# Performance work log

Hardware: AMD Instinct MI355X
Metric: run time of the kernel (lower is better)

The kernel has to match this reference:

```python
import jax, jax.numpy as jnp
import numpy as np

DIM = 2048
HEADS = 16
B = 2
T = 2048


def setup_inputs() -> dict:
    key = jax.random.key(0)
    k_x, k_qkv, k_out, k_b = jax.random.split(key, 4)
    inv = DIM ** -0.5
    return {
        "x": jax.random.normal(k_x, (B, T, DIM), dtype=jnp.float32),
        "w_qkv": jax.random.normal(k_qkv, (DIM, 3 * DIM), dtype=jnp.float32) * inv,
        "w_out": jax.random.normal(k_out, (DIM, DIM), dtype=jnp.float32) * inv,
        "b_out": jnp.zeros((DIM,), dtype=jnp.float32),
    }


def reference(x, w_qkv, w_out, b_out):
    b, t, e = x.shape
    h = HEADS
    d = e // h
    scale = d ** -0.5
    qkv = x @ w_qkv                              # [b, t, 3e]
    q, k, v = jnp.split(qkv, 3, axis=-1)
    # [b, t, e] -> [b, h, t, d]
    q, k, v = (a.reshape(b, t, h, d).transpose(0, 2, 1, 3) for a in (q, k, v))
    dots = jnp.einsum("bhid,bhjd->bhij", q, k) * scale  # [b, h, t, t]
    causal_mask = jnp.triu(jnp.ones((t, t), dtype=bool), k=1)  # True where j > i
    dots = jnp.where(causal_mask[None, None, :, :], -jnp.inf, dots)
    attn = jax.nn.softmax(dots, axis=-1)
    out = jnp.einsum("bhij,bhjd->bhid", attn, v)  # [b, h, t, d]
    out = out.transpose(0, 2, 1, 3).reshape(b, t, e)
    return out @ w_out + b_out
```

## Files before the change

### kernel.cpp

```cpp
#include <hip/hip_runtime.h>
#include <stdint.h>

#define BATCH 2
#define TDIM 2048
#define EDIM 2048
#define NH 16
#define HD 128
#define E3 6144
#define MROWS 4096

typedef short v8bf __attribute__((ext_vector_type(8)));
typedef float v4f  __attribute__((ext_vector_type(4)));

typedef __attribute__((address_space(3))) uint8_t lds_u8;
typedef __attribute__((address_space(1))) uint8_t glb_u8;

__device__ __forceinline__ void gload16(const void* g, void* l) {
    __builtin_amdgcn_global_load_lds((const glb_u8*)g, (lds_u8*)l, 16, 0, 0);
}

__device__ __forceinline__ ushort f2bf(float f) {
    uint32_t u = __float_as_uint(f);
    return (ushort)((u + 0x7fffu + ((u >> 16) & 1u)) >> 16);
}

__global__ void cvtx_kernel(const float* __restrict__ in, ushort* __restrict__ out, int n) {
    int i = (blockIdx.x * 256 + threadIdx.x) * 4;
    const int stride = gridDim.x * 256 * 4;
    for (; i < n; i += stride) {
        const float4 v = *reinterpret_cast<const float4*>(in + i);
        ushort4 o = make_ushort4(f2bf(v.x), f2bf(v.y), f2bf(v.z), f2bf(v.w));
        *reinterpret_cast<ushort4*>(out + i) = o;
    }
}

__global__ void tcvt_kernel(const float* __restrict__ in, ushort* __restrict__ out, int R, int C) {
    __shared__ float t[32][33];
    const int tc = blockIdx.x * 32;
    const int tr = blockIdx.y * 32;
    const int tid = threadIdx.x;
    const int row = tid >> 3, c4 = (tid & 7) * 4;
    const float4 v = *reinterpret_cast<const float4*>(in + (size_t)(tr + row) * C + tc + c4);
    t[row][c4] = v.x; t[row][c4 + 1] = v.y; t[row][c4 + 2] = v.z; t[row][c4 + 3] = v.w;
    __syncthreads();
    const int oc = tid >> 3, r4 = (tid & 7) * 4;
    ushort4 o = make_ushort4(f2bf(t[r4][oc]), f2bf(t[r4 + 1][oc]),
                             f2bf(t[r4 + 2][oc]), f2bf(t[r4 + 3][oc]));
    *reinterpret_cast<ushort4*>(out + (size_t)(tc + oc) * R + tr + r4) = o;
}

__global__ void vtrans_kernel(const ushort* __restrict__ qkv, ushort* __restrict__ vt) {
    __shared__ ushort t[32][33];
    const int bh = blockIdx.z;
    const int b = bh >> 4, h = bh & 15;
    const int tr = blockIdx.x * 32;
    const int tc = blockIdx.y * 32;
    const int tid = threadIdx.x;
    const int row = tid >> 3, c4 = (tid & 7) * 4;
    const ushort4 v = *reinterpret_cast<const ushort4*>(
        qkv + (size_t)(b * TDIM + tr + row) * E3 + 2 * EDIM + h * HD + tc + c4);
    t[row][c4] = v.x; t[row][c4 + 1] = v.y; t[row][c4 + 2] = v.z; t[row][c4 + 3] = v.w;
    __syncthreads();
    const int oc = tid >> 3, r4 = (tid & 7) * 4;
    ushort4 o = make_ushort4(t[r4][oc], t[r4 + 1][oc], t[r4 + 2][oc], t[r4 + 3][oc]);
    *reinterpret_cast<ushort4*>(vt + (size_t)(bh * HD + tc + oc) * TDIM + tr + r4) = o;
}

template <int OUTF32>
__global__ void gemm_kernel(const ushort* __restrict__ A, const ushort* __restrict__ Bt,
                            void* __restrict__ Cv, const float* __restrict__ bias,
                            int Mdim, int Ndim, int Kdim) {
    __shared__ __align__(16) ushort As[128 * 64];
    __shared__ __align__(16) ushort Bs[128 * 64];
    const int tid = threadIdx.x;
    const int lane = tid & 63;
    const int wv = tid >> 6;
    const int l4 = lane >> 4, l16 = lane & 15;
    const int nbn = Ndim >> 7;
    const int nwg = (Mdim >> 7) * nbn;
    int bid = blockIdx.x;
    bid = (bid & 7) * (nwg >> 3) + (bid >> 3);
    const int bm = bid / nbn, bn = bid % nbn;
    const int wr = wv >> 1, wc = wv & 1;

    const ushort* Abase = A + (size_t)(bm * 128) * Kdim;
    const ushort* Bbase = Bt + (size_t)(bn * 128) * Kdim;

    v4f acc[4][4] = {};

    for (int k0 = 0; k0 < Kdim; k0 += 64) {
#pragma unroll
        for (int i = 0; i < 4; ++i) {
            const int c = i * 256 + tid;
            const int row = c >> 3;
            const int kc = (c & 7) ^ (row & 7);
            gload16(Abase + (size_t)row * Kdim + k0 + kc * 8, &As[(i * 256 + wv * 64) * 8]);
        }
#pragma unroll
        for (int i = 0; i < 4; ++i) {
            const int c = i * 256 + tid;
            const int row = c >> 3;
            const int kc = (c & 7) ^ (row & 7);
            gload16(Bbase + (size_t)row * Kdim + k0 + kc * 8, &Bs[(i * 256 + wv * 64) * 8]);
        }
        __syncthreads();
#pragma unroll
        for (int kk = 0; kk < 2; ++kk) {
            v8bf af[4], bfr[4];
#pragma unroll
            for (int m = 0; m < 4; ++m) {
                const int r = wr * 64 + m * 16 + l16;
                const int slot = (kk * 4 + l4) ^ (r & 7);
                af[m] = *reinterpret_cast<const v8bf*>(&As[r * 64 + slot * 8]);
            }
#pragma unroll
            for (int n = 0; n < 4; ++n) {
                const int r = wc * 64 + n * 16 + l16;
                const int slot = (kk * 4 + l4) ^ (r & 7);
                bfr[n] = *reinterpret_cast<const v8bf*>(&Bs[r * 64 + slot * 8]);
            }
#pragma unroll
            for (int m = 0; m < 4; ++m)
#pragma unroll
                for (int n = 0; n < 4; ++n)
                    acc[m][n] = __builtin_amdgcn_mfma_f32_16x16x32_bf16(af[m], bfr[n], acc[m][n], 0, 0, 0);
        }
        __syncthreads();
    }

    const int r0 = bm * 128 + wr * 64 + l4 * 4;
    const int c0 = bn * 128 + wc * 64 + l16;
    if (OUTF32) {
        float* C = (float*)Cv;
#pragma unroll
        for (int n = 0; n < 4; ++n) {
            const float bv = bias[c0 + n * 16];
#pragma unroll
            for (int m = 0; m < 4; ++m)
#pragma unroll
                for (int j = 0; j < 4; ++j)
                    C[(size_t)(r0 + m * 16 + j) * Ndim + c0 + n * 16] = acc[m][n][j] + bv;
        }
    } else {
        ushort* C = (ushort*)Cv;
#pragma unroll
        for (int n = 0; n < 4; ++n)
#pragma unroll
            for (int m = 0; m < 4; ++m)
#pragma unroll
                for (int j = 0; j < 4; ++j)
                    C[(size_t)(r0 + m * 16 + j) * Ndim + c0 + n * 16] = f2bf(acc[m][n][j]);
    }
}

__global__ __launch_bounds__(256, 2) void flash_kernel(const ushort* __restrict__ qkv,
                                                       const ushort* __restrict__ vt,
                                                       ushort* __restrict__ ao) {
    __shared__ __align__(16) ushort Kl[2][64 * 128];
    __shared__ __align__(16) ushort Vl[2][128 * 64];
    __shared__ __align__(16) ushort Pl[128 * 64];

    const int qt = (TDIM / 128 - 1) - blockIdx.x;
    const int h = blockIdx.y;
    const int b = blockIdx.z;
    const int tid = threadIdx.x;
    const int lane = tid & 63;
    const int wv = tid >> 6;
    const int l4 = lane >> 4, l16 = lane & 15;
    const int q0 = qt * 128;

    v8bf qf[2][4];
#pragma unroll
    for (int mg = 0; mg < 2; ++mg) {
        const ushort* qp = qkv + (size_t)(b * TDIM + q0 + wv * 32 + mg * 16 + l16) * E3 + h * HD + l4 * 8;
#pragma unroll
        for (int d0 = 0; d0 < 4; ++d0)
            qf[mg][d0] = *reinterpret_cast<const v8bf*>(qp + d0 * 32);
    }

    float mrun[2][4], lrun[2][4];
#pragma unroll
    for (int mg = 0; mg < 2; ++mg)
#pragma unroll
        for (int j = 0; j < 4; ++j) { mrun[mg][j] = -1e30f; lrun[mg][j] = 0.0f; }
    v4f oacc[2][8] = {};

    const ushort* kbase = qkv + (size_t)(b * TDIM) * E3 + EDIM + h * HD;
    const ushort* vbase = vt + (size_t)((b * 16 + h) * HD) * TDIM;
    const int nkt = 2 * qt + 2;

#define STAGE(BUF, KT)                                                                        \
    do {                                                                                      \
        _Pragma("unroll") for (int i = 0; i < 4; ++i) {                                       \
            const int c = i * 256 + tid;                                                      \
            const int row = c >> 4;                                                           \
            const int dc = (c & 15) ^ (row & 7);                                              \
            gload16(kbase + (size_t)((KT) * 64 + row) * E3 + dc * 8,                          \
                    &Kl[BUF][(i * 256 + wv * 64) * 8]);                                       \
        }                                                                                     \
        _Pragma("unroll") for (int i = 0; i < 4; ++i) {                                       \
            const int c = i * 256 + tid;                                                      \
            const int row = c >> 3;                                                           \
            const int jc = (c & 7) ^ (row & 7);                                               \
            gload16(vbase + (size_t)row * TDIM + (KT) * 64 + jc * 8,                          \
                    &Vl[BUF][(i * 256 + wv * 64) * 8]);                                       \
        }                                                                                     \
    } while (0)

    STAGE(0, 0);
    __syncthreads();
    int cur = 0;

    for (int kt = 0; kt < nkt; ++kt) {
        if (kt + 1 < nkt) STAGE(cur ^ 1, kt + 1);

        const ushort* Kb = &Kl[cur][0];
        const ushort* Vb = &Vl[cur][0];

        v4f s[2][4] = {};
#pragma unroll
        for (int d0 = 0; d0 < 4; ++d0) {
            v8bf kf[4];
#pragma unroll
            for (int kvn = 0; kvn < 4; ++kvn) {
                const int r = kvn * 16 + l16;
                const int slot = (d0 * 4 + l4) ^ (r & 7);
                kf[kvn] = *reinterpret_cast<const v8bf*>(&Kb[r * 128 + slot * 8]);
            }
#pragma unroll
            for (int mg = 0; mg < 2; ++mg)
#pragma unroll
                for (int kvn = 0; kvn < 4; ++kvn)
                    s[mg][kvn] = __builtin_amdgcn_mfma_f32_16x16x32_bf16(qf[mg][d0], kf[kvn], s[mg][kvn], 0, 0, 0);
        }

        float sv[2][4][4];
#pragma unroll
        for (int mg = 0; mg < 2; ++mg)
#pragma unroll
            for (int kvn = 0; kvn < 4; ++kvn)
#pragma unroll
                for (int j = 0; j < 4; ++j)
                    sv[mg][kvn][j] = s[mg][kvn][j] * 0.08838834764831845f;

        if (kt >= 2 * qt) {
#pragma unroll
            for (int mg = 0; mg < 2; ++mg) {
                const int rg = q0 + wv * 32 + mg * 16 + l4 * 4;
#pragma unroll
                for (int kvn = 0; kvn < 4; ++kvn) {
                    const int cg = kt * 64 + kvn * 16 + l16;
#pragma unroll
                    for (int j = 0; j < 4; ++j)
                        if (cg > rg + j) sv[mg][kvn][j] = -__builtin_inff();
                }
            }
        }

        float p[2][4][4];
#pragma unroll
        for (int mg = 0; mg < 2; ++mg) {
            float corr[4];
#pragma unroll
            for (int j = 0; j < 4; ++j) {
                float pm = fmaxf(fmaxf(sv[mg][0][j], sv[mg][1][j]), fmaxf(sv[mg][2][j], sv[mg][3][j]));
                pm = fmaxf(pm, __shfl_xor(pm, 1));
                pm = fmaxf(pm, __shfl_xor(pm, 2));
                pm = fmaxf(pm, __shfl_xor(pm, 4));
                pm = fmaxf(pm, __shfl_xor(pm, 8));
                const float mn = fmaxf(mrun[mg][j], pm);
                corr[j] = __expf(mrun[mg][j] - mn);
                mrun[mg][j] = mn;
            }
#pragma unroll
            for (int kvn = 0; kvn < 4; ++kvn)
#pragma unroll
                for (int j = 0; j < 4; ++j)
                    p[mg][kvn][j] = __expf(sv[mg][kvn][j] - mrun[mg][j]);
#pragma unroll
            for (int j = 0; j < 4; ++j)
                lrun[mg][j] = lrun[mg][j] * corr[j] + p[mg][0][j] + p[mg][1][j] + p[mg][2][j] + p[mg][3][j];
#pragma unroll
            for (int n = 0; n < 8; ++n)
#pragma unroll
                for (int j = 0; j < 4; ++j)
                    oacc[mg][n][j] *= corr[j];
        }

#pragma unroll
        for (int mg = 0; mg < 2; ++mg) {
            const int row = wv * 32 + mg * 16 + l4 * 4;
#pragma unroll
            for (int kvn = 0; kvn < 4; ++kvn) {
                const int cc = kvn * 2 + (l16 >> 3);
#pragma unroll
                for (int j = 0; j < 4; ++j) {
                    const int r = row + j;
                    Pl[r * 64 + ((cc ^ (r & 7)) * 8) + (l16 & 7)] = f2bf(p[mg][kvn][j]);
                }
            }
        }

#pragma unroll
        for (int kk = 0; kk < 2; ++kk) {
            v8bf pf[2];
#pragma unroll
            for (int mg = 0; mg < 2; ++mg) {
                const int r = wv * 32 + mg * 16 + l16;
                const int slot = (kk * 4 + l4) ^ (r & 7);
                pf[mg] = *reinterpret_cast<const v8bf*>(&Pl[r * 64 + slot * 8]);
            }
#pragma unroll
            for (int n = 0; n < 8; ++n) {
                const int dr = n * 16 + l16;
                const int slot = (kk * 4 + l4) ^ (dr & 7);
                v8bf vf = *reinterpret_cast<const v8bf*>(&Vb[dr * 64 + slot * 8]);
#pragma unroll
                for (int mg = 0; mg < 2; ++mg)
                    oacc[mg][n] = __builtin_amdgcn_mfma_f32_16x16x32_bf16(pf[mg], vf, oacc[mg][n], 0, 0, 0);
            }
        }
        __syncthreads();
        cur ^= 1;
    }
#undef STAGE

#pragma unroll
    for (int mg = 0; mg < 2; ++mg) {
        float inv[4];
#pragma unroll
        for (int j = 0; j < 4; ++j) {
            float l = lrun[mg][j];
            l += __shfl_xor(l, 1);
            l += __shfl_xor(l, 2);
            l += __shfl_xor(l, 4);
            l += __shfl_xor(l, 8);
            inv[j] = 1.0f / l;
        }
        ushort* aop = ao + (size_t)(b * TDIM + q0 + wv * 32 + mg * 16 + l4 * 4) * EDIM + h * HD + l16;
#pragma unroll
        for (int n = 0; n < 8; ++n)
#pragma unroll
            for (int j = 0; j < 4; ++j)
                aop[(size_t)j * EDIM + n * 16] = f2bf(oacc[mg][n][j] * inv[j]);
    }
}

extern "C" void kernel_launch(void* const* d_in, const int* in_sizes, int n_in,
                              void* d_out, int out_size, void* d_ws, size_t ws_size,
                              hipStream_t stream) {
    (void)in_sizes; (void)n_in; (void)out_size; (void)ws_size;
    const float* x     = (const float*)d_in[0];
    const float* w_qkv = (const float*)d_in[1];
    const float* w_out = (const float*)d_in[2];
    const float* b_out = (const float*)d_in[3];

    uint8_t* ws = (uint8_t*)d_ws;
    ushort* qkv   = (ushort*)(ws);
    ushort* woutT = (ushort*)(ws + 50331648u);
    ushort* xb    = (ushort*)(ws + 58720256u);
    ushort* wqkvT = (ushort*)(ws + 75497472u);
    ushort* vtb   = xb;
    ushort* ao    = wqkvT;

    cvtx_kernel<<<2048, 256, 0, stream>>>(x, xb, MROWS * EDIM);
    tcvt_kernel<<<dim3(E3 / 32, EDIM / 32), 256, 0, stream>>>(w_qkv, wqkvT, EDIM, E3);
    tcvt_kernel<<<dim3(EDIM / 32, EDIM / 32), 256, 0, stream>>>(w_out, woutT, EDIM, EDIM);

    gemm_kernel<0><<<(MROWS / 128) * (E3 / 128), 256, 0, stream>>>(
        xb, wqkvT, (void*)qkv, nullptr, MROWS, E3, EDIM);

    vtrans_kernel<<<dim3(TDIM / 32, HD / 32, BATCH * NH), 256, 0, stream>>>(qkv, vtb);

    flash_kernel<<<dim3(TDIM / 128, NH, BATCH), 256, 0, stream>>>(qkv, vtb, ao);

    gemm_kernel<1><<<(MROWS / 128) * (EDIM / 128), 256, 0, stream>>>(
        ao, woutT, d_out, b_out, MROWS, EDIM, EDIM);
}
```

Before: 298.8 us.

## Pair mirrored causal query tiles per block and use lazy softmax rescaling

Result: faster. 265.1 us (-11.3%).

```diff
diff --git a/kernel.cpp b/kernel.cpp
--- a/kernel.cpp
+++ b/kernel.cpp
@@ -160,22 +160,34 @@
     __shared__ __align__(16) ushort Vl[2][128 * 64];
     __shared__ __align__(16) ushort Pl[128 * 64];
 
-    const int qt = (TDIM / 128 - 1) - blockIdx.x;
+    const int xi = blockIdx.x;
+    const int ti = (xi & 1) ? (xi >> 1) : (15 - (xi >> 1));
     const int h = blockIdx.y;
     const int b = blockIdx.z;
     const int tid = threadIdx.x;
     const int lane = tid & 63;
     const int wv = tid >> 6;
     const int l4 = lane >> 4, l16 = lane & 15;
-    const int q0 = qt * 128;
+
+    const int rbs[2]  = {ti * 64 + wv * 16, TDIM - 64 * (ti + 1) + wv * 16};
+    const int diag[2] = {ti, 31 - ti};
+    const int nkt = 32 - ti;
 
     v8bf qf[2][4];
 #pragma unroll
     for (int mg = 0; mg < 2; ++mg) {
-        const ushort* qp = qkv + (size_t)(b * TDIM + q0 + wv * 32 + mg * 16 + l16) * E3 + h * HD + l4 * 8;
-#pragma unroll
-        for (int d0 = 0; d0 < 4; ++d0)
-            qf[mg][d0] = *reinterpret_cast<const v8bf*>(qp + d0 * 32);
+        const ushort* qp = qkv + (size_t)(b * TDIM + rbs[mg] + l16) * E3 + h * HD + l4 * 8;
+#pragma unroll
+        for (int d0 = 0; d0 < 4; ++d0) {
+            v8bf r = *reinterpret_cast<const v8bf*>(qp + d0 * 32);
+            v8bf o;
+#pragma unroll
+            for (int e = 0; e < 8; ++e) {
+                const float f = __uint_as_float(((uint32_t)(ushort)r[e]) << 16) * 0.08838834764831845f;
+                o[e] = (short)f2bf(f);
+            }
+            qf[mg][d0] = o;
+        }
     }
 
     float mrun[2][4], lrun[2][4];
@@ -187,7 +199,6 @@
 
     const ushort* kbase = qkv + (size_t)(b * TDIM) * E3 + EDIM + h * HD;
     const ushort* vbase = vt + (size_t)((b * 16 + h) * HD) * TDIM;
-    const int nkt = 2 * qt + 2;
 
 #define STAGE(BUF, KT)                                                                        \
     do {                                                                                      \
@@ -214,6 +225,7 @@
     for (int kt = 0; kt < nkt; ++kt) {
         if (kt + 1 < nkt) STAGE(cur ^ 1, kt + 1);
 
+        const bool act0 = (kt <= diag[0]);
         const ushort* Kb = &Kl[cur][0];
         const ushort* Vb = &Vl[cur][0];
 
@@ -228,67 +240,72 @@
                 kf[kvn] = *reinterpret_cast<const v8bf*>(&Kb[r * 128 + slot * 8]);
             }
 #pragma unroll
-            for (int mg = 0; mg < 2; ++mg)
-#pragma unroll
-                for (int kvn = 0; kvn < 4; ++kvn)
-                    s[mg][kvn] = __builtin_amdgcn_mfma_f32_16x16x32_bf16(qf[mg][d0], kf[kvn], s[mg][kvn], 0, 0, 0);
-        }
-
-        float sv[2][4][4];
-#pragma unroll
-        for (int mg = 0; mg < 2; ++mg)
+            for (int kvn = 0; kvn < 4; ++kvn) {
+                if (act0)
+                    s[0][kvn] = __builtin_amdgcn_mfma_f32_16x16x32_bf16(qf[0][d0], kf[kvn], s[0][kvn], 0, 0, 0);
+                s[1][kvn] = __builtin_amdgcn_mfma_f32_16x16x32_bf16(qf[1][d0], kf[kvn], s[1][kvn], 0, 0, 0);
+            }
+        }
+
+#pragma unroll
+        for (int mg = 0; mg < 2; ++mg) {
+            if (mg == 0 && !act0) continue;
+
+            float sv[4][4];
 #pragma unroll
             for (int kvn = 0; kvn < 4; ++kvn)
 #pragma unroll
                 for (int j = 0; j < 4; ++j)
-                    sv[mg][kvn][j] = s[mg][kvn][j] * 0.08838834764831845f;
-
-        if (kt >= 2 * qt) {
-#pragma unroll
-            for (int mg = 0; mg < 2; ++mg) {
-                const int rg = q0 + wv * 32 + mg * 16 + l4 * 4;
+                    sv[kvn][j] = s[mg][kvn][j];
+
+            if (kt == diag[mg]) {
+                const int rg = rbs[mg] + l4 * 4;
 #pragma unroll
                 for (int kvn = 0; kvn < 4; ++kvn) {
                     const int cg = kt * 64 + kvn * 16 + l16;
 #pragma unroll
                     for (int j = 0; j < 4; ++j)
-                        if (cg > rg + j) sv[mg][kvn][j] = -__builtin_inff();
+                        if (cg > rg + j) sv[kvn][j] = -__builtin_inff();
                 }
             }
-        }
-
-        float p[2][4][4];
-#pragma unroll
-        for (int mg = 0; mg < 2; ++mg) {
-            float corr[4];
+
+            float pm[4], dmax = -1e30f;
 #pragma unroll
             for (int j = 0; j < 4; ++j) {
-                float pm = fmaxf(fmaxf(sv[mg][0][j], sv[mg][1][j]), fmaxf(sv[mg][2][j], sv[mg][3][j]));
-                pm = fmaxf(pm, __shfl_xor(pm, 1));
-                pm = fmaxf(pm, __shfl_xor(pm, 2));
-                pm = fmaxf(pm, __shfl_xor(pm, 4));
-                pm = fmaxf(pm, __shfl_xor(pm, 8));
-                const float mn = fmaxf(mrun[mg][j], pm);
-                corr[j] = __expf(mrun[mg][j] - mn);
-                mrun[mg][j] = mn;
-            }
+                float m0 = fmaxf(fmaxf(sv[0][j], sv[1][j]), fmaxf(sv[2][j], sv[3][j]));
+                m0 = fmaxf(m0, __shfl_xor(m0, 1));
+                m0 = fmaxf(m0, __shfl_xor(m0, 2));
+                m0 = fmaxf(m0, __shfl_xor(m0, 4));
+                m0 = fmaxf(m0, __shfl_xor(m0, 8));
+                pm[j] = m0;
+                dmax = fmaxf(dmax, m0 - mrun[mg][j]);
+            }
+            if (!__all(dmax <= 8.0f)) {
+                float corr[4];
+#pragma unroll
+                for (int j = 0; j < 4; ++j) {
+                    const float mn = fmaxf(mrun[mg][j], pm[j]);
+                    corr[j] = __expf(mrun[mg][j] - mn);
+                    mrun[mg][j] = mn;
+                    lrun[mg][j] *= corr[j];
+                }
+#pragma unroll
+                for (int n = 0; n < 8; ++n)
+#pragma unroll
+                    for (int j = 0; j < 4; ++j)
+                        oacc[mg][n][j] *= corr[j];
+            }
+
+            float p[4][4];
 #pragma unroll
             for (int kvn = 0; kvn < 4; ++kvn)
 #pragma unroll
                 for (int j = 0; j < 4; ++j)
-                    p[mg][kvn][j] = __expf(sv[mg][kvn][j] - mrun[mg][j]);
+                    p[kvn][j] = __expf(sv[kvn][j] - mrun[mg][j]);
 #pragma unroll
             for (int j = 0; j < 4; ++j)
-                lrun[mg][j] = lrun[mg][j] * corr[j] + p[mg][0][j] + p[mg][1][j] + p[mg][2][j] + p[mg][3][j];
-#pragma unroll
-            for (int n = 0; n < 8; ++n)
-#pragma unroll
-                for (int j = 0; j < 4; ++j)
-                    oacc[mg][n][j] *= corr[j];
-        }
-
-#pragma unroll
-        for (int mg = 0; mg < 2; ++mg) {
+                lrun[mg][j] += p[0][j] + p[1][j] + p[2][j] + p[3][j];
+
             const int row = wv * 32 + mg * 16 + l4 * 4;
 #pragma unroll
             for (int kvn = 0; kvn < 4; ++kvn) {
@@ -296,7 +313,7 @@
 #pragma unroll
                 for (int j = 0; j < 4; ++j) {
                     const int r = row + j;
-                    Pl[r * 64 + ((cc ^ (r & 7)) * 8) + (l16 & 7)] = f2bf(p[mg][kvn][j]);
+                    Pl[r * 64 + ((cc ^ (r & 7)) * 8) + (l16 & 7)] = f2bf(p[kvn][j]);
                 }
             }
         }
@@ -306,6 +323,7 @@
             v8bf pf[2];
 #pragma unroll
             for (int mg = 0; mg < 2; ++mg) {
+                if (mg == 0 && !act0) continue;
                 const int r = wv * 32 + mg * 16 + l16;
                 const int slot = (kk * 4 + l4) ^ (r & 7);
                 pf[mg] = *reinterpret_cast<const v8bf*>(&Pl[r * 64 + slot * 8]);
@@ -315,9 +333,9 @@
                 const int dr = n * 16 + l16;
                 const int slot = (kk * 4 + l4) ^ (dr & 7);
                 v8bf vf = *reinterpret_cast<const v8bf*>(&Vb[dr * 64 + slot * 8]);
-#pragma unroll
-                for (int mg = 0; mg < 2; ++mg)
-                    oacc[mg][n] = __builtin_amdgcn_mfma_f32_16x16x32_bf16(pf[mg], vf, oacc[mg][n], 0, 0, 0);
+                if (act0)
+                    oacc[0][n] = __builtin_amdgcn_mfma_f32_16x16x32_bf16(pf[0], vf, oacc[0][n], 0, 0, 0);
+                oacc[1][n] = __builtin_amdgcn_mfma_f32_16x16x32_bf16(pf[1], vf, oacc[1][n], 0, 0, 0);
             }
         }
         __syncthreads();
@@ -337,7 +355,7 @@
             l += __shfl_xor(l, 8);
             inv[j] = 1.0f / l;
         }
-        ushort* aop = ao + (size_t)(b * TDIM + q0 + wv * 32 + mg * 16 + l4 * 4) * EDIM + h * HD + l16;
+        ushort* aop = ao + (size_t)(b * TDIM + rbs[mg] + l4 * 4) * EDIM + h * HD + l16;
 #pragma unroll
         for (int n = 0; n < 8; ++n)
 #pragma unroll
@@ -372,7 +390,7 @@
 
     vtrans_kernel<<<dim3(TDIM / 32, HD / 32, BATCH * NH), 256, 0, stream>>>(qkv, vtb);
 
-    flash_kernel<<<dim3(TDIM / 128, NH, BATCH), 256, 0, stream>>>(qkv, vtb, ao);
+    flash_kernel<<<dim3(16, NH, BATCH), 256, 0, stream>>>(qkv, vtb, ao);
 
     gemm_kernel<1><<<(MROWS / 128) * (EDIM / 128), 256, 0, stream>>>(
         ao, woutT, d_out, b_out, MROWS, EDIM, EDIM);
```
